# Kernel optimization log

Measured on AMD Instinct MI355X. Metric: run time of the kernel, lower is better.

Reference implementation:

```python
import jax, jax.numpy as jnp
import numpy as np

B, C, N = 8, 768, 256
H = 12            # num_heads[0]
D = C // H        # head_dim = 64


def setup_inputs() -> dict:
    key = jax.random.key(0)
    ks = jax.random.split(key, 4)
    s = 0.02
    return {
        "x_ori": jax.random.normal(ks[0], (B, C, N), jnp.float32),
        "cross": jax.random.normal(ks[1], (B, C, N), jnp.float32),
        "W_proj": jax.random.normal(ks[2], (C, C), jnp.float32) * s,
        "b_proj": jnp.zeros((C,), jnp.float32),
        "W_dep": jax.random.normal(ks[3], (C, C), jnp.float32) * s,
        "b_dep": jnp.zeros((C,), jnp.float32),
    }


def reference(x_ori, cross, W_proj, b_proj, W_dep, b_dep):
    # x_ori, cross: [B, C, N] with channel axis factored as (head_dim D, num_heads H)
    Bn, Cn, Nn = x_ori.shape
    Nc = cross.shape[-1]
    scale = D ** (-0.5)

    # 'B (d H) N -> B d (H N)'
    x = x_ori.reshape(Bn, D, H, Nn).reshape(Bn, D, H * Nn)

    # proj over channel axis (1x1 conv): [B, C, Nc]
    cp = jnp.einsum('oc,bcn->bon', W_proj, cross) + b_proj[None, :, None]
    cp = cp.reshape(Bn, D, H, Nc).reshape(Bn, D, H * Nc)      # 'B (d H) Nc -> B d (H Nc)'

    # 'B (d H) Nc -> B (H Nc) d'
    cr = cross.reshape(Bn, D, H, Nc).transpose(0, 2, 3, 1).reshape(Bn, H * Nc, D)

    # raw attention (no softmax in original source)
    atten = jnp.einsum('bdm,bdn->bmn', x, cp) * scale          # [B, H*N, H*Nc]
    out = jnp.einsum('bmn,bnd->bmd', atten, cr)                # [B, H*N, D]

    # 'B (N H) d -> B N (H d)'  (note (num, head) grouping per source)
    out = out.reshape(Bn, Nn, H, D).reshape(Bn, Nn, H * D)

    y = out @ W_dep.T + b_dep                                  # deproj: [B, N, C]
    # skip connection (dropout is identity at eval / drop_ratio=0)
    return x_ori + y.transpose(0, 2, 1)
```

## Files before the change

### kernel.cpp

```cpp
#include <hip/hip_runtime.h>

typedef unsigned short u16;
typedef short bf16x8 __attribute__((ext_vector_type(8)));
typedef float f32x4 __attribute__((ext_vector_type(4)));

#define BB 8
#define CC 768
#define NN 256
#define HH 12
#define DD 64
#define K3 3072
#define BCN 196608
#define SCALE 0.125f
#define LDP 72

__device__ __forceinline__ u16 f2b(float f) {
    union { float f; unsigned int i; } v; v.f = f;
    unsigned int r = v.i + 0x7FFFu + ((v.i >> 16) & 1u);
    return (u16)(r >> 16);
}

#define MFMA8(ASP, BSP, ACC)                                                              \
    _Pragma("unroll")                                                                     \
    for (int kk = 0; kk < 2; ++kk) {                                                      \
        bf16x8 a0 = *reinterpret_cast<bf16x8*>((ASP) + (wm + tx) * LDP + kk * 32 + q * 8);\
        bf16x8 a1 = *reinterpret_cast<bf16x8*>((ASP) + (wm + 16 + tx) * LDP + kk * 32 + q * 8);\
        bf16x8 b0 = *reinterpret_cast<bf16x8*>((BSP) + (wn + tx) * LDP + kk * 32 + q * 8);\
        bf16x8 b1 = *reinterpret_cast<bf16x8*>((BSP) + (wn + 16 + tx) * LDP + kk * 32 + q * 8);\
        ACC[0][0] = __builtin_amdgcn_mfma_f32_16x16x32_bf16(a0, b0, ACC[0][0], 0, 0, 0);  \
        ACC[0][1] = __builtin_amdgcn_mfma_f32_16x16x32_bf16(a0, b1, ACC[0][1], 0, 0, 0);  \
        ACC[1][0] = __builtin_amdgcn_mfma_f32_16x16x32_bf16(a1, b0, ACC[1][0], 0, 0, 0);  \
        ACC[1][1] = __builtin_amdgcn_mfma_f32_16x16x32_bf16(a1, b1, ACC[1][1], 0, 0, 0);  \
    }

__global__ __launch_bounds__(256) void k_proj(
    const float* __restrict__ Wp, const float* __restrict__ cross,
    const float* __restrict__ bp, u16* __restrict__ cp, float* __restrict__ G)
{
    __shared__ __align__(16) u16 As[64 * LDP];
    __shared__ __align__(16) u16 Bs[64 * LDP];
    __shared__ __align__(16) float T[64][68];
    const int n0 = blockIdx.x * 64;
    const int o0 = blockIdx.y * 64;
    const int b  = blockIdx.z;
    const int t = threadIdx.x;
    const int lane = t & 63, wave = t >> 6;
    const int q = lane >> 4, tx = lane & 15;
    const int wm = (wave & 1) * 32, wn = (wave >> 1) * 32;
    const int r4 = t >> 2, cq = t & 3;

    if (blockIdx.x == 0 && blockIdx.y == 0) {
        float4 z = {0.f, 0.f, 0.f, 0.f};
        float* Gb = G + b * 4096;
        #pragma unroll
        for (int j = 0; j < 4; ++j)
            *reinterpret_cast<float4*>(Gb + t * 4 + j * 1024) = z;
    }

    const float* crb = cross + b * BCN;
    const float* wsrc = Wp + (o0 + r4) * CC;

    f32x4 acc[2][2] = {};
    float4 ra[4], rc[4];
    #pragma unroll
    for (int u = 0; u < 4; ++u) {
        const int cl = (cq + 4 * u) * 4;
        ra[u] = *reinterpret_cast<const float4*>(wsrc + cl);
        rc[u] = *reinterpret_cast<const float4*>(crb + r4 * NN + n0 + cl);
    }
    for (int it = 0; it < 12; ++it) {
        if (it > 0) __syncthreads();
        {
            u16* dstA = As + r4 * LDP;
            #pragma unroll
            for (int u = 0; u < 4; ++u) {
                const int cl = (cq + 4 * u) * 4;
                ushort4 w; w.x = f2b(ra[u].x); w.y = f2b(ra[u].y);
                w.z = f2b(ra[u].z); w.w = f2b(ra[u].w);
                *reinterpret_cast<ushort4*>(dstA + cl) = w;
                T[r4][cl + 0] = rc[u].x; T[r4][cl + 1] = rc[u].y;
                T[r4][cl + 2] = rc[u].z; T[r4][cl + 3] = rc[u].w;
            }
        }
        if (it < 11) {
            const int c0 = (it + 1) * 64;
            #pragma unroll
            for (int u = 0; u < 4; ++u) {
                const int cl = (cq + 4 * u) * 4;
                ra[u] = *reinterpret_cast<const float4*>(wsrc + c0 + cl);
                rc[u] = *reinterpret_cast<const float4*>(crb + (c0 + r4) * NN + n0 + cl);
            }
        }
        __syncthreads();
        {
            const int nn = t >> 2, dq = t & 3;
            u16* dst = Bs + nn * LDP;
            #pragma unroll
            for (int u = 0; u < 4; ++u) {
                const int c4 = (dq + 4 * u) * 4;
                ushort4 w;
                w.x = f2b(T[c4 + 0][nn]); w.y = f2b(T[c4 + 1][nn]);
                w.z = f2b(T[c4 + 2][nn]); w.w = f2b(T[c4 + 3][nn]);
                *reinterpret_cast<ushort4*>(dst + c4) = w;
            }
        }
        __syncthreads();
        MFMA8(As, Bs, acc)
    }
    u16* cpb = cp + b * BCN;
    #pragma unroll
    for (int i = 0; i < 2; ++i)
        #pragma unroll
        for (int j = 0; j < 2; ++j)
            #pragma unroll
            for (int r = 0; r < 4; ++r) {
                const int o = o0 + wm + i * 16 + q * 4 + r;
                const int n = n0 + wn + j * 16 + tx;
                cpb[o * NN + n] = f2b(acc[i][j][r] + bp[o]);
            }
}

__global__ __launch_bounds__(256) void k_gram(
    const float* __restrict__ cross, const u16* __restrict__ cp, float* __restrict__ G)
{
    __shared__ __align__(16) u16 As[64 * LDP];
    __shared__ __align__(16) u16 Bs[64 * LDP];
    const int kb = blockIdx.x * 64;
    const int b  = blockIdx.y;
    const int t = threadIdx.x;
    const int lane = t & 63, wave = t >> 6;
    const int q = lane >> 4, tx = lane & 15;
    const int wm = (wave & 1) * 32, wn = (wave >> 1) * 32;
    const float* crb = cross + b * BCN;
    const u16* cpb = cp + b * BCN;
    f32x4 acc[2][2] = {};
    {
        const int r = t >> 2, cq = t & 3;
        const float* src = crb + r * K3 + kb;
        u16* dst = As + r * LDP;
        #pragma unroll
        for (int u = 0; u < 4; ++u) {
            const int cl = (cq + 4 * u) * 4;
            float4 v = *reinterpret_cast<const float4*>(src + cl);
            ushort4 w; w.x = f2b(v.x); w.y = f2b(v.y); w.z = f2b(v.z); w.w = f2b(v.w);
            *reinterpret_cast<ushort4*>(dst + cl) = w;
        }
    }
    {
        const int r = t >> 3, ch = (t & 7) * 8;
        *reinterpret_cast<uint4*>(Bs + r * LDP + ch) =
            *reinterpret_cast<const uint4*>(cpb + r * K3 + kb + ch);
        *reinterpret_cast<uint4*>(Bs + (r + 32) * LDP + ch) =
            *reinterpret_cast<const uint4*>(cpb + (r + 32) * K3 + kb + ch);
    }
    __syncthreads();
    MFMA8(As, Bs, acc)
    float* Gb = G + b * 4096;
    #pragma unroll
    for (int i = 0; i < 2; ++i)
        #pragma unroll
        for (int j = 0; j < 2; ++j)
            #pragma unroll
            for (int r = 0; r < 4; ++r) {
                const int dd = wm + i * 16 + q * 4 + r;
                const int d  = wn + j * 16 + tx;
                atomicAdd(Gb + dd * DD + d, acc[i][j][r] * SCALE);
            }
}

__global__ __launch_bounds__(256) void k_xm(
    const float* __restrict__ x, const float* __restrict__ G, u16* __restrict__ U)
{
    __shared__ __align__(16) u16 As[64 * LDP];
    __shared__ __align__(16) u16 Bs[64 * LDP];
    __shared__ __align__(16) float T[64][68];
    const int m0 = blockIdx.x * 64;
    const int b  = blockIdx.y;
    const int h   = m0 >> 8;
    const int nn0 = m0 & 255;
    const int t = threadIdx.x;
    const int lane = t & 63, wave = t >> 6;
    const int q = lane >> 4, tx = lane & 15;
    const int wm = (wave & 1) * 32, wn = (wave >> 1) * 32;
    const float* xb = x + b * BCN;
    const float* Gb = G + b * 4096;
    f32x4 acc[2][2] = {};
    {
        const int d = t >> 2, fq = t & 3;
        const float* src = xb + (d * HH + h) * NN + nn0;
        #pragma unroll
        for (int u = 0; u < 4; ++u) {
            const int nl = (fq + 4 * u) * 4;
            float4 v = *reinterpret_cast<const float4*>(src + nl);
            T[d][nl + 0] = v.x; T[d][nl + 1] = v.y; T[d][nl + 2] = v.z; T[d][nl + 3] = v.w;
        }
    }
    {
        const int r = t >> 2, cq = t & 3;
        const float* src = Gb + r * DD;
        u16* dst = Bs + r * LDP;
        #pragma unroll
        for (int u = 0; u < 4; ++u) {
            const int cl = (cq + 4 * u) * 4;
            float4 v = *reinterpret_cast<const float4*>(src + cl);
            ushort4 w; w.x = f2b(v.x); w.y = f2b(v.y); w.z = f2b(v.z); w.w = f2b(v.w);
            *reinterpret_cast<ushort4*>(dst + cl) = w;
        }
    }
    __syncthreads();
    {
        const int nn = t >> 2, dq = t & 3;
        u16* dst = As + nn * LDP;
        #pragma unroll
        for (int u = 0; u < 4; ++u) {
            const int d4 = (dq + 4 * u) * 4;
            ushort4 w;
            w.x = f2b(T[d4 + 0][nn]); w.y = f2b(T[d4 + 1][nn]);
            w.z = f2b(T[d4 + 2][nn]); w.w = f2b(T[d4 + 3][nn]);
            *reinterpret_cast<ushort4*>(dst + d4) = w;
        }
    }
    __syncthreads();
    MFMA8(As, Bs, acc)
    u16* Ub = U + b * BCN;
    #pragma unroll
    for (int i = 0; i < 2; ++i)
        #pragma unroll
        for (int j = 0; j < 2; ++j)
            #pragma unroll
            for (int r = 0; r < 4; ++r) {
                const int m  = m0 + wm + i * 16 + q * 4 + r;
                const int dd = wn + j * 16 + tx;
                Ub[m * DD + dd] = f2b(acc[i][j][r]);
            }
}

__global__ __launch_bounds__(256) void k_dep(
    const float* __restrict__ Wd, const u16* __restrict__ U,
    const float* __restrict__ bd, const float* __restrict__ x, float* __restrict__ out)
{
    __shared__ __align__(16) u16 As[64 * LDP];
    __shared__ __align__(16) u16 Bs[64 * LDP];
    const int n0 = blockIdx.x * 64;
    const int o0 = blockIdx.y * 64;
    const int b  = blockIdx.z;
    const int t = threadIdx.x;
    const int lane = t & 63, wave = t >> 6;
    const int q = lane >> 4, tx = lane & 15;
    const int wm = (wave & 1) * 32, wn = (wave >> 1) * 32;
    const int r4 = t >> 2, cq = t & 3;
    const int r8 = t >> 3, ch = (t & 7) * 8;
    const u16* Ub = U + b * BCN;
    const float* srcA0 = Wd + (o0 + r4) * CC;

    float4 ra[4]; uint4 rb[2];
    #pragma unroll
    for (int u = 0; u < 4; ++u)
        ra[u] = *reinterpret_cast<const float4*>(srcA0 + (cq + 4 * u) * 4);
    rb[0] = *reinterpret_cast<const uint4*>(Ub + (n0 + r8) * CC + ch);
    rb[1] = *reinterpret_cast<const uint4*>(Ub + (n0 + r8 + 32) * CC + ch);

    f32x4 acc[2][2] = {};
    for (int it = 0; it < 12; ++it) {
        if (it > 0) __syncthreads();
        {
            u16* dst = As + r4 * LDP;
            #pragma unroll
            for (int u = 0; u < 4; ++u) {
                const int cl = (cq + 4 * u) * 4;
                ushort4 w; w.x = f2b(ra[u].x); w.y = f2b(ra[u].y);
                w.z = f2b(ra[u].z); w.w = f2b(ra[u].w);
                *reinterpret_cast<ushort4*>(dst + cl) = w;
            }
            *reinterpret_cast<uint4*>(Bs + r8 * LDP + ch) = rb[0];
            *reinterpret_cast<uint4*>(Bs + (r8 + 32) * LDP + ch) = rb[1];
        }
        if (it < 11) {
            const int c0 = (it + 1) * 64;
            #pragma unroll
            for (int u = 0; u < 4; ++u)
                ra[u] = *reinterpret_cast<const float4*>(srcA0 + c0 + (cq + 4 * u) * 4);
            rb[0] = *reinterpret_cast<const uint4*>(Ub + (n0 + r8) * CC + c0 + ch);
            rb[1] = *reinterpret_cast<const uint4*>(Ub + (n0 + r8 + 32) * CC + c0 + ch);
        }
        __syncthreads();
        MFMA8(As, Bs, acc)
    }
    #pragma unroll
    for (int i = 0; i < 2; ++i)
        #pragma unroll
        for (int j = 0; j < 2; ++j)
            #pragma unroll
            for (int r = 0; r < 4; ++r) {
                const int o = o0 + wm + i * 16 + q * 4 + r;
                const int n = n0 + wn + j * 16 + tx;
                const int idx = b * BCN + o * NN + n;
                out[idx] = acc[i][j][r] + bd[o] + x[idx];
            }
}

extern "C" void kernel_launch(void* const* d_in, const int* in_sizes, int n_in,
                              void* d_out, int out_size, void* d_ws, size_t ws_size,
                              hipStream_t stream) {
    const float* x_ori = (const float*)d_in[0];
    const float* cross = (const float*)d_in[1];
    const float* Wp    = (const float*)d_in[2];
    const float* bp    = (const float*)d_in[3];
    const float* Wd    = (const float*)d_in[4];
    const float* bd    = (const float*)d_in[5];
    float* out = (float*)d_out;

    u16*   cp = (u16*)d_ws;
    u16*   U  = (u16*)d_ws;
    float* G  = (float*)((char*)d_ws + (size_t)BB * BCN * sizeof(u16));

    k_proj<<<dim3(4, 12, BB), 256, 0, stream>>>(Wp, cross, bp, cp, G);
    k_gram<<<dim3(48, BB), 256, 0, stream>>>(cross, cp, G);
    k_xm  <<<dim3(48, BB), 256, 0, stream>>>(x_ori, G, U);
    k_dep <<<dim3(4, 12, BB), 256, 0, stream>>>(Wd, U, bd, x_ori, out);
}
```

Measured before the change: 118.2 us.

## Fuse gram and x-times-G kernels with a per-batch grid spin barrier

Merges the Gram-accumulation kernel and the x·G kernel into one launch. Each batch's 48 blocks first atomically accumulate into G, then increment a per-batch counter and spin until all 48 have arrived before computing U. The counter is reset inside k_proj. This removes one kernel launch and the gap between launches. It depends on all blocks of a batch being resident at once, and it adds spin-wait and atomic-fence overhead.

```diff
diff --git a/kernel.cpp b/kernel.cpp
--- a/kernel.cpp
+++ b/kernel.cpp
@@ -35,7 +35,8 @@
 
 __global__ __launch_bounds__(256) void k_proj(
     const float* __restrict__ Wp, const float* __restrict__ cross,
-    const float* __restrict__ bp, u16* __restrict__ cp, float* __restrict__ G)
+    const float* __restrict__ bp, u16* __restrict__ cp, float* __restrict__ G,
+    unsigned int* __restrict__ Cnt)
 {
     __shared__ __align__(16) u16 As[64 * LDP];
     __shared__ __align__(16) u16 Bs[64 * LDP];
@@ -55,6 +56,7 @@
         #pragma unroll
         for (int j = 0; j < 4; ++j)
             *reinterpret_cast<float4*>(Gb + t * 4 + j * 1024) = z;
+        if (t == 0) Cnt[b] = 0u;
     }
 
     const float* crb = cross + b * BCN;
@@ -120,119 +122,123 @@
             }
 }
 
-__global__ __launch_bounds__(256) void k_gram(
-    const float* __restrict__ cross, const u16* __restrict__ cp, float* __restrict__ G)
+__global__ __launch_bounds__(256) void k_gx(
+    const float* __restrict__ cross, u16* __restrict__ cpU,
+    const float* __restrict__ x, float* __restrict__ G,
+    unsigned int* __restrict__ Cnt)
 {
     __shared__ __align__(16) u16 As[64 * LDP];
     __shared__ __align__(16) u16 Bs[64 * LDP];
-    const int kb = blockIdx.x * 64;
-    const int b  = blockIdx.y;
+    __shared__ __align__(16) float T[64][68];
+    const int r = blockIdx.x;
+    const int b = blockIdx.y;
     const int t = threadIdx.x;
     const int lane = t & 63, wave = t >> 6;
     const int q = lane >> 4, tx = lane & 15;
     const int wm = (wave & 1) * 32, wn = (wave >> 1) * 32;
-    const float* crb = cross + b * BCN;
-    const u16* cpb = cp + b * BCN;
-    f32x4 acc[2][2] = {};
+    float* Gb = G + b * 4096;
+
     {
-        const int r = t >> 2, cq = t & 3;
-        const float* src = crb + r * K3 + kb;
-        u16* dst = As + r * LDP;
-        #pragma unroll
-        for (int u = 0; u < 4; ++u) {
-            const int cl = (cq + 4 * u) * 4;
-            float4 v = *reinterpret_cast<const float4*>(src + cl);
-            ushort4 w; w.x = f2b(v.x); w.y = f2b(v.y); w.z = f2b(v.z); w.w = f2b(v.w);
-            *reinterpret_cast<ushort4*>(dst + cl) = w;
-        }
-    }
+        const int kb = r * 64;
+        const float* crb = cross + b * BCN;
+        const u16* cpb = cpU + b * BCN;
+        f32x4 acc[2][2] = {};
+        {
+            const int rr = t >> 2, cq = t & 3;
+            const float* src = crb + rr * K3 + kb;
+            u16* dst = As + rr * LDP;
+            #pragma unroll
+            for (int u = 0; u < 4; ++u) {
+                const int cl = (cq + 4 * u) * 4;
+                float4 v = *reinterpret_cast<const float4*>(src + cl);
+                ushort4 w; w.x = f2b(v.x); w.y = f2b(v.y); w.z = f2b(v.z); w.w = f2b(v.w);
+                *reinterpret_cast<ushort4*>(dst + cl) = w;
+            }
+        }
+        {
+            const int rr = t >> 3, ch = (t & 7) * 8;
+            *reinterpret_cast<uint4*>(Bs + rr * LDP + ch) =
+                *reinterpret_cast<const uint4*>(cpb + rr * K3 + kb + ch);
+            *reinterpret_cast<uint4*>(Bs + (rr + 32) * LDP + ch) =
+                *reinterpret_cast<const uint4*>(cpb + (rr + 32) * K3 + kb + ch);
+        }
+        __syncthreads();
+        MFMA8(As, Bs, acc)
+        #pragma unroll
+        for (int i = 0; i < 2; ++i)
+            #pragma unroll
+            for (int j = 0; j < 2; ++j)
+                #pragma unroll
+                for (int rr = 0; rr < 4; ++rr) {
+                    const int dd = wm + i * 16 + q * 4 + rr;
+                    const int d  = wn + j * 16 + tx;
+                    atomicAdd(Gb + dd * DD + d, acc[i][j][rr] * SCALE);
+                }
+    }
+
+    __syncthreads();
+    if (t == 0) {
+        __hip_atomic_fetch_add(&Cnt[b], 1u, __ATOMIC_RELEASE, __HIP_MEMORY_SCOPE_AGENT);
+        while (__hip_atomic_load(&Cnt[b], __ATOMIC_ACQUIRE, __HIP_MEMORY_SCOPE_AGENT) < 48u)
+            __builtin_amdgcn_s_sleep(8);
+    }
+    __syncthreads();
+
     {
-        const int r = t >> 3, ch = (t & 7) * 8;
-        *reinterpret_cast<uint4*>(Bs + r * LDP + ch) =
-            *reinterpret_cast<const uint4*>(cpb + r * K3 + kb + ch);
-        *reinterpret_cast<uint4*>(Bs + (r + 32) * LDP + ch) =
-            *reinterpret_cast<const uint4*>(cpb + (r + 32) * K3 + kb + ch);
-    }
-    __syncthreads();
-    MFMA8(As, Bs, acc)
-    float* Gb = G + b * 4096;
-    #pragma unroll
-    for (int i = 0; i < 2; ++i)
-        #pragma unroll
-        for (int j = 0; j < 2; ++j)
-            #pragma unroll
-            for (int r = 0; r < 4; ++r) {
-                const int dd = wm + i * 16 + q * 4 + r;
-                const int d  = wn + j * 16 + tx;
-                atomicAdd(Gb + dd * DD + d, acc[i][j][r] * SCALE);
-            }
-}
-
-__global__ __launch_bounds__(256) void k_xm(
-    const float* __restrict__ x, const float* __restrict__ G, u16* __restrict__ U)
-{
-    __shared__ __align__(16) u16 As[64 * LDP];
-    __shared__ __align__(16) u16 Bs[64 * LDP];
-    __shared__ __align__(16) float T[64][68];
-    const int m0 = blockIdx.x * 64;
-    const int b  = blockIdx.y;
-    const int h   = m0 >> 8;
-    const int nn0 = m0 & 255;
-    const int t = threadIdx.x;
-    const int lane = t & 63, wave = t >> 6;
-    const int q = lane >> 4, tx = lane & 15;
-    const int wm = (wave & 1) * 32, wn = (wave >> 1) * 32;
-    const float* xb = x + b * BCN;
-    const float* Gb = G + b * 4096;
-    f32x4 acc[2][2] = {};
-    {
-        const int d = t >> 2, fq = t & 3;
-        const float* src = xb + (d * HH + h) * NN + nn0;
-        #pragma unroll
-        for (int u = 0; u < 4; ++u) {
-            const int nl = (fq + 4 * u) * 4;
-            float4 v = *reinterpret_cast<const float4*>(src + nl);
-            T[d][nl + 0] = v.x; T[d][nl + 1] = v.y; T[d][nl + 2] = v.z; T[d][nl + 3] = v.w;
-        }
-    }
-    {
-        const int r = t >> 2, cq = t & 3;
-        const float* src = Gb + r * DD;
-        u16* dst = Bs + r * LDP;
-        #pragma unroll
-        for (int u = 0; u < 4; ++u) {
-            const int cl = (cq + 4 * u) * 4;
-            float4 v = *reinterpret_cast<const float4*>(src + cl);
-            ushort4 w; w.x = f2b(v.x); w.y = f2b(v.y); w.z = f2b(v.z); w.w = f2b(v.w);
-            *reinterpret_cast<ushort4*>(dst + cl) = w;
-        }
-    }
-    __syncthreads();
-    {
-        const int nn = t >> 2, dq = t & 3;
-        u16* dst = As + nn * LDP;
-        #pragma unroll
-        for (int u = 0; u < 4; ++u) {
-            const int d4 = (dq + 4 * u) * 4;
-            ushort4 w;
-            w.x = f2b(T[d4 + 0][nn]); w.y = f2b(T[d4 + 1][nn]);
-            w.z = f2b(T[d4 + 2][nn]); w.w = f2b(T[d4 + 3][nn]);
-            *reinterpret_cast<ushort4*>(dst + d4) = w;
-        }
-    }
-    __syncthreads();
-    MFMA8(As, Bs, acc)
-    u16* Ub = U + b * BCN;
-    #pragma unroll
-    for (int i = 0; i < 2; ++i)
-        #pragma unroll
-        for (int j = 0; j < 2; ++j)
-            #pragma unroll
-            for (int r = 0; r < 4; ++r) {
-                const int m  = m0 + wm + i * 16 + q * 4 + r;
-                const int dd = wn + j * 16 + tx;
-                Ub[m * DD + dd] = f2b(acc[i][j][r]);
-            }
+        const int m0 = r * 64;
+        const int h   = m0 >> 8;
+        const int nn0 = m0 & 255;
+        const float* xb = x + b * BCN;
+        f32x4 acc[2][2] = {};
+        {
+            const int d = t >> 2, fq = t & 3;
+            const float* src = xb + (d * HH + h) * NN + nn0;
+            #pragma unroll
+            for (int u = 0; u < 4; ++u) {
+                const int nl = (fq + 4 * u) * 4;
+                float4 v = *reinterpret_cast<const float4*>(src + nl);
+                T[d][nl + 0] = v.x; T[d][nl + 1] = v.y; T[d][nl + 2] = v.z; T[d][nl + 3] = v.w;
+            }
+        }
+        {
+            const int rr = t >> 2, cq = t & 3;
+            const float* src = Gb + rr * DD;
+            u16* dst = Bs + rr * LDP;
+            #pragma unroll
+            for (int u = 0; u < 4; ++u) {
+                const int cl = (cq + 4 * u) * 4;
+                float4 v = *reinterpret_cast<const float4*>(src + cl);
+                ushort4 w; w.x = f2b(v.x); w.y = f2b(v.y); w.z = f2b(v.z); w.w = f2b(v.w);
+                *reinterpret_cast<ushort4*>(dst + cl) = w;
+            }
+        }
+        __syncthreads();
+        {
+            const int nn = t >> 2, dq = t & 3;
+            u16* dst = As + nn * LDP;
+            #pragma unroll
+            for (int u = 0; u < 4; ++u) {
+                const int d4 = (dq + 4 * u) * 4;
+                ushort4 w;
+                w.x = f2b(T[d4 + 0][nn]); w.y = f2b(T[d4 + 1][nn]);
+                w.z = f2b(T[d4 + 2][nn]); w.w = f2b(T[d4 + 3][nn]);
+                *reinterpret_cast<ushort4*>(dst + d4) = w;
+            }
+        }
+        __syncthreads();
+        MFMA8(As, Bs, acc)
+        u16* Ub = cpU + b * BCN;
+        #pragma unroll
+        for (int i = 0; i < 2; ++i)
+            #pragma unroll
+            for (int j = 0; j < 2; ++j)
+                #pragma unroll
+                for (int rr = 0; rr < 4; ++rr) {
+                    const int m  = m0 + wm + i * 16 + q * 4 + rr;
+                    const int dd = wn + j * 16 + tx;
+                    Ub[m * DD + dd] = f2b(acc[i][j][rr]);
+                }
+    }
 }
 
 __global__ __launch_bounds__(256) void k_dep(
@@ -311,11 +317,11 @@
     float* out = (float*)d_out;
 
     u16*   cp = (u16*)d_ws;
-    u16*   U  = (u16*)d_ws;
     float* G  = (float*)((char*)d_ws + (size_t)BB * BCN * sizeof(u16));
-
-    k_proj<<<dim3(4, 12, BB), 256, 0, stream>>>(Wp, cross, bp, cp, G);
-    k_gram<<<dim3(48, BB), 256, 0, stream>>>(cross, cp, G);
-    k_xm  <<<dim3(48, BB), 256, 0, stream>>>(x_ori, G, U);
-    k_dep <<<dim3(4, 12, BB), 256, 0, stream>>>(Wd, U, bd, x_ori, out);
-}
+    unsigned int* Cnt = (unsigned int*)((char*)d_ws + (size_t)BB * BCN * sizeof(u16)
+                                        + (size_t)BB * DD * DD * sizeof(float));
+
+    k_proj<<<dim3(4, 12, BB), 256, 0, stream>>>(Wp, cross, bp, cp, G, Cnt);
+    k_gx  <<<dim3(48, BB), 256, 0, stream>>>(cross, cp, x_ori, G, Cnt);
+    k_dep <<<dim3(4, 12, BB), 256, 0, stream>>>(Wd, cp, bd, x_ori, out);
+}
```

Result: slower. 133.7 us (+13.0%).
